# Kernel tuning notes

Measured on AMD Instinct MI355X. Metric: run time of the kernel, lower is better.

Reference implementation:

```python
import jax, jax.numpy as jnp
import numpy as np

HIDDEN = 2048
N_HEADS = 16
N_KV_HEADS = 4
HEAD_DIM = HIDDEN // N_HEADS  # 128
N_GROUPS = N_HEADS // N_KV_HEADS  # 4
ROPE_BASE = 10000.0


def rope_cos_sin(seq_len, dim, dtype=jnp.float32):
    inv_freq = 1.0 / (ROPE_BASE ** (jnp.arange(0, dim, 2, dtype=jnp.float32) / dim))
    t = jnp.arange(seq_len, dtype=jnp.float32)
    freqs = jnp.einsum('i,j->ij', t, inv_freq)          # [S, dim/2]
    emb = jnp.concatenate([freqs, freqs], axis=-1)       # [S, dim]
    return emb.astype(dtype).cos(), emb.astype(dtype).sin() if False else (jnp.cos(emb).astype(dtype), jnp.sin(emb).astype(dtype))[1] and None or (jnp.cos(emb).astype(dtype), jnp.sin(emb).astype(dtype))


def _rope_tables(seq_len, dim):
    inv_freq = 1.0 / (ROPE_BASE ** (jnp.arange(0, dim, 2, dtype=jnp.float32) / dim))
    t = jnp.arange(seq_len, dtype=jnp.float32)
    freqs = jnp.einsum('i,j->ij', t, inv_freq)
    emb = jnp.concatenate([freqs, freqs], axis=-1)
    return jnp.cos(emb), jnp.sin(emb)  # each [S, dim]


def rotate_half(x):
    d = x.shape[-1] // 2
    return jnp.concatenate([-x[..., d:], x[..., :d]], axis=-1)


def setup_inputs() -> dict:
    key = jax.random.key(0)
    ks = jax.random.split(key, 5)
    B, S = 2, 2048
    std = 0.02
    return {
        'hidden_states': jax.random.normal(ks[0], (B, S, HIDDEN), jnp.float32),
        'wq': jax.random.normal(ks[1], (HIDDEN, N_HEADS * HEAD_DIM), jnp.float32) * std,
        'wk': jax.random.normal(ks[2], (HIDDEN, N_KV_HEADS * HEAD_DIM), jnp.float32) * std,
        'wv': jax.random.normal(ks[3], (HIDDEN, N_KV_HEADS * HEAD_DIM), jnp.float32) * std,
        'wo': jax.random.normal(ks[4], (HIDDEN, HIDDEN), jnp.float32) * std,
    }


def reference(hidden_states, wq, wk, wv, wo):
    B, S, _ = hidden_states.shape
    q = (hidden_states @ wq).reshape(B, S, N_HEADS, HEAD_DIM)       # [B,S,Hq,D]
    k = (hidden_states @ wk).reshape(B, S, N_KV_HEADS, HEAD_DIM)    # [B,S,Hk,D]
    v = (hidden_states @ wv).reshape(B, S, N_KV_HEADS, HEAD_DIM)

    cos, sin = _rope_tables(S, HEAD_DIM)                            # [S,D]
    cos = cos[None, :, None, :]
    sin = sin[None, :, None, :]
    q = q * cos + rotate_half(q) * sin
    k = k * cos + rotate_half(k) * sin

    # GQA: repeat KV heads so kv head h maps to query heads h*G..h*G+G-1
    # (matches einops repeat 'b h s d -> b (h g) s d')
    k = jnp.repeat(k, N_GROUPS, axis=2)                              # [B,S,Hq,D]
    v = jnp.repeat(v, N_GROUPS, axis=2)

    scale = 1.0 / jnp.sqrt(jnp.asarray(HEAD_DIM, q.dtype))
    scores = jnp.einsum('bqhd,bkhd->bhqk', q, k) * scale            # [B,H,S,S]
    causal = jnp.triu(jnp.full((S, S), -jnp.inf, dtype=scores.dtype), k=1)
    scores = scores + causal
    probs = jax.nn.softmax(scores.astype(jnp.float32), axis=-1).astype(q.dtype)
    out = jnp.einsum('bhqk,bkhd->bqhd', probs, v)                   # [B,S,H,D]
    out = out.reshape(B, S, HIDDEN)
    return out @ wo
```

## Files before the change

kernel.cpp:

```cpp
#include <hip/hip_runtime.h>

#define HIDDEN 2048
#define NH 16
#define NKV 4
#define HD 128
#define BATCH 2
#define SEQ 2048
#define MROWS (BATCH*SEQ)
#define NQKV (NH*HD + 2*NKV*HD)
#define KOFF (NH*HD)
#define VOFF (NH*HD + NKV*HD)

typedef unsigned short u16;
typedef unsigned int u32;
typedef __bf16 bf16_t;
typedef bf16_t bf16x8 __attribute__((ext_vector_type(8)));
typedef float f32x4 __attribute__((ext_vector_type(4)));
typedef u16 u16x8 __attribute__((ext_vector_type(8)));

__device__ __forceinline__ u16 f2bf(float f) {
  u32 u = __builtin_bit_cast(u32, f);
  u32 r = (u + 0x7FFFu + ((u >> 16) & 1u)) >> 16;
  return (u16)r;
}
__device__ __forceinline__ float bf2f(u16 h) {
  u32 u = ((u32)h) << 16;
  return __builtin_bit_cast(float, u);
}

__global__ void cast_f32_bf16(const float* __restrict__ in, u16* __restrict__ out, int n8) {
  int i = blockIdx.x * blockDim.x + threadIdx.x;
  if (i >= n8) return;
  const float4* p = (const float4*)in + (size_t)i * 2;
  float4 a = p[0], b = p[1];
  u16x8 o;
  o[0]=f2bf(a.x); o[1]=f2bf(a.y); o[2]=f2bf(a.z); o[3]=f2bf(a.w);
  o[4]=f2bf(b.x); o[5]=f2bf(b.y); o[6]=f2bf(b.z); o[7]=f2bf(b.w);
  *((u16x8*)out + i) = o;
}

__global__ void transpose_cast(const float* __restrict__ src, u16* __restrict__ dst, int K, int N) {
  __shared__ float tile[32][33];
  int k0 = blockIdx.y * 32, n0 = blockIdx.x * 32;
  int tx = threadIdx.x, ty = threadIdx.y;
  #pragma unroll
  for (int j = 0; j < 32; j += 8)
    tile[ty + j][tx] = src[(size_t)(k0 + ty + j) * N + n0 + tx];
  __syncthreads();
  #pragma unroll
  for (int j = 0; j < 32; j += 8)
    dst[(size_t)(n0 + ty + j) * K + k0 + tx] = f2bf(tile[tx][ty + j]);
}

template<int OUT_BF16>
__global__ __launch_bounds__(256) void gemm_bt(const u16* __restrict__ A, const u16* __restrict__ Bt,
                                               void* __restrict__ Cout, int M, int N, int K) {
  __shared__ u16 As[2][128 * 32];
  __shared__ u16 Bs[2][128 * 32];
  const int tid = threadIdx.x;
  const int lane = tid & 63, wave = tid >> 6;
  const int mb = blockIdx.y * 128, nb = blockIdx.x * 128;
  const int wm = (wave >> 1) * 64, wn = (wave & 1) * 64;
  const int KT = K >> 5;

  auto stage = [&](int buf, int kt) {
    #pragma unroll
    for (int j = 0; j < 2; ++j) {
      int id0 = j * 256 + wave * 64;
      int id = id0 + lane;
      int row = id >> 2, c8 = (id & 3) * 8;
      const u16* ga = A + (size_t)(mb + row) * K + kt * 32 + c8;
      __builtin_amdgcn_global_load_lds((const __attribute__((address_space(1))) u32*)ga,
          (__attribute__((address_space(3))) u32*)&As[buf][id0 * 8], 16, 0, 0);
      const u16* gb = Bt + (size_t)(nb + row) * K + kt * 32 + c8;
      __builtin_amdgcn_global_load_lds((const __attribute__((address_space(1))) u32*)gb,
          (__attribute__((address_space(3))) u32*)&Bs[buf][id0 * 8], 16, 0, 0);
    }
  };

  f32x4 acc[4][4];
  #pragma unroll
  for (int i = 0; i < 4; ++i)
    #pragma unroll
    for (int j = 0; j < 4; ++j) acc[i][j] = (f32x4)0.0f;

  stage(0, 0);
  __syncthreads();
  for (int kt = 0; kt < KT; ++kt) {
    int cur = kt & 1;
    if (kt + 1 < KT) stage(cur ^ 1, kt + 1);
    bf16x8 af[4], bfr[4];
    #pragma unroll
    for (int mi = 0; mi < 4; ++mi) {
      int r = wm + mi * 16 + (lane & 15);
      af[mi] = __builtin_bit_cast(bf16x8, *(const u16x8*)&As[cur][r * 32 + (lane >> 4) * 8]);
    }
    #pragma unroll
    for (int ni = 0; ni < 4; ++ni) {
      int r = wn + ni * 16 + (lane & 15);
      bfr[ni] = __builtin_bit_cast(bf16x8, *(const u16x8*)&Bs[cur][r * 32 + (lane >> 4) * 8]);
    }
    #pragma unroll
    for (int mi = 0; mi < 4; ++mi)
      #pragma unroll
      for (int ni = 0; ni < 4; ++ni)
        acc[mi][ni] = __builtin_amdgcn_mfma_f32_16x16x32_bf16(af[mi], bfr[ni], acc[mi][ni], 0, 0, 0);
    __syncthreads();
  }
  int rbase = mb + wm + (lane >> 4) * 4;
  int cbase = nb + wn + (lane & 15);
  #pragma unroll
  for (int mi = 0; mi < 4; ++mi) {
    #pragma unroll
    for (int r = 0; r < 4; ++r) {
      int row = rbase + mi * 16 + r;
      #pragma unroll
      for (int ni = 0; ni < 4; ++ni) {
        int col = cbase + ni * 16;
        float v = acc[mi][ni][r];
        if (OUT_BF16) ((u16*)Cout)[(size_t)row * N + col] = f2bf(v);
        else          ((float*)Cout)[(size_t)row * N + col] = v;
      }
    }
  }
}

__global__ void rope_kernel(u16* __restrict__ qkv) {
  int idx = blockIdx.x * blockDim.x + threadIdx.x;
  int d = idx & 63;
  int t = idx >> 6;
  int hd = t % 20;
  int row = t / 20;
  int s = row & (SEQ - 1);
  int cb = (hd < NH) ? hd * HD : KOFF + (hd - NH) * HD;
  float inv = __expf((float)d * -0.14391156f);
  float freq = (float)s * inv;
  float sn = sinf(freq), cs = cosf(freq);
  size_t base = (size_t)row * NQKV + cb + d;
  float x0 = bf2f(qkv[base]), x1 = bf2f(qkv[base + 64]);
  qkv[base]      = f2bf(x0 * cs - x1 * sn);
  qkv[base + 64] = f2bf(x1 * cs + x0 * sn);
}

__global__ void vtrans_kernel(const u16* __restrict__ qkv, u16* __restrict__ vt) {
  __shared__ u16 tile[32][33];
  int bh = blockIdx.z;
  int d0 = blockIdx.y * 32;
  int s0 = blockIdx.x * 32;
  int b = bh >> 2, kvh = bh & 3;
  int tx = threadIdx.x, ty = threadIdx.y;
  const u16* src = qkv + (size_t)(b * SEQ) * NQKV + VOFF + kvh * HD;
  #pragma unroll
  for (int j = 0; j < 32; j += 8)
    tile[ty + j][tx] = src[(size_t)(s0 + ty + j) * NQKV + d0 + tx];
  __syncthreads();
  u16* dst = vt + (size_t)bh * HD * SEQ;
  #pragma unroll
  for (int j = 0; j < 32; j += 8)
    dst[(size_t)(d0 + ty + j) * SEQ + s0 + tx] = tile[tx][ty + j];
}

__global__ __launch_bounds__(512) void attn_kernel(const u16* __restrict__ qkv,
                                                   const u16* __restrict__ vt,
                                                   u16* __restrict__ out) {
  __shared__ u16 Ks[32 * 128];
  __shared__ u16 Vs[128 * 32];
  __shared__ u16 Ps[8][16 * 32];
  const int tid = threadIdx.x, lane = tid & 63, wave = tid >> 6;
  const int qt = blockIdx.x, h = blockIdx.y, b = blockIdx.z;
  const int kvh = h >> 2;
  const int q0 = qt * 128 + wave * 16;
  const float scale = 0.08838834764831845f;

  bf16x8 qf[4];
  {
    const u16* qp = qkv + (size_t)(b * SEQ + q0 + (lane & 15)) * NQKV + h * HD + (lane >> 4) * 8;
    #pragma unroll
    for (int kc = 0; kc < 4; ++kc)
      qf[kc] = __builtin_bit_cast(bf16x8, *(const u16x8*)(qp + kc * 32));
  }
  f32x4 oacc[8];
  #pragma unroll
  for (int i = 0; i < 8; ++i) oacc[i] = (f32x4)0.0f;
  float mrow[4], lrow[4];
  #pragma unroll
  for (int r = 0; r < 4; ++r) { mrow[r] = -INFINITY; lrow[r] = 0.0f; }

  const int ntiles = (qt + 1) * 4;
  const u16* kbase = qkv + (size_t)(b * SEQ) * NQKV + KOFF + kvh * HD;
  const u16* vbase = vt + (size_t)(b * NKV + kvh) * HD * SEQ;

  for (int t = 0; t < ntiles; ++t) {
    int kv0 = t * 32;
    {
      int row = tid >> 4, c8 = (tid & 15) * 8;
      u16x8 kd = *(const u16x8*)(kbase + (size_t)(kv0 + row) * NQKV + c8);
      int byte = (row * 256 + c8 * 2) ^ ((row & 7) << 4);
      *(u16x8*)((char*)Ks + byte) = kd;
      int vrow = tid >> 2, vc8 = (tid & 3) * 8;
      u16x8 vd = *(const u16x8*)(vbase + (size_t)vrow * SEQ + kv0 + vc8);
      int vbyte = (vrow * 64 + vc8 * 2) ^ ((vrow & 3) << 4);
      *(u16x8*)((char*)Vs + vbyte) = vd;
    }
    __syncthreads();
    if (kv0 <= q0 + 15) {
      f32x4 sacc[2];
      sacc[0] = (f32x4)0.0f; sacc[1] = (f32x4)0.0f;
      #pragma unroll
      for (int n2 = 0; n2 < 2; ++n2) {
        #pragma unroll
        for (int kc = 0; kc < 4; ++kc) {
          int kvr = n2 * 16 + (lane & 15);
          int byte = (kvr * 256 + (kc * 32 + (lane >> 4) * 8) * 2) ^ ((kvr & 7) << 4);
          bf16x8 kf = __builtin_bit_cast(bf16x8, *(const u16x8*)((const char*)Ks + byte));
          sacc[n2] = __builtin_amdgcn_mfma_f32_16x16x32_bf16(qf[kc], kf, sacc[n2], 0, 0, 0);
        }
      }
      int qrow_base = q0 + (lane >> 4) * 4;
      float pv[2][4];
      #pragma unroll
      for (int r = 0; r < 4; ++r) {
        int q = qrow_base + r;
        #pragma unroll
        for (int n2 = 0; n2 < 2; ++n2) {
          int kv = kv0 + n2 * 16 + (lane & 15);
          float sv = sacc[n2][r] * scale;
          pv[n2][r] = (kv <= q) ? sv : -INFINITY;
        }
        float v = fmaxf(pv[0][r], pv[1][r]);
        v = fmaxf(v, __shfl_xor(v, 1));
        v = fmaxf(v, __shfl_xor(v, 2));
        v = fmaxf(v, __shfl_xor(v, 4));
        v = fmaxf(v, __shfl_xor(v, 8));
        float mnew = fmaxf(mrow[r], v);
        float corr = __expf(mrow[r] - mnew);
        mrow[r] = mnew;
        float psum = 0.0f;
        #pragma unroll
        for (int n2 = 0; n2 < 2; ++n2) {
          float p = __expf(pv[n2][r] - mnew);
          pv[n2][r] = p;
          psum += p;
        }
        psum += __shfl_xor(psum, 1);
        psum += __shfl_xor(psum, 2);
        psum += __shfl_xor(psum, 4);
        psum += __shfl_xor(psum, 8);
        lrow[r] = lrow[r] * corr + psum;
        #pragma unroll
        for (int nt = 0; nt < 8; ++nt) oacc[nt][r] *= corr;
      }
      #pragma unroll
      for (int n2 = 0; n2 < 2; ++n2)
        #pragma unroll
        for (int r = 0; r < 4; ++r)
          Ps[wave][((lane >> 4) * 4 + r) * 32 + n2 * 16 + (lane & 15)] = f2bf(pv[n2][r]);
      asm volatile("s_waitcnt lgkmcnt(0)" ::: "memory");
      bf16x8 pf = __builtin_bit_cast(bf16x8, *(const u16x8*)&Ps[wave][(lane & 15) * 32 + (lane >> 4) * 8]);
      #pragma unroll
      for (int nt = 0; nt < 8; ++nt) {
        int d = nt * 16 + (lane & 15);
        int vbyte = (d * 64 + (lane >> 4) * 16) ^ ((d & 3) << 4);
        bf16x8 vf = __builtin_bit_cast(bf16x8, *(const u16x8*)((const char*)Vs + vbyte));
        oacc[nt] = __builtin_amdgcn_mfma_f32_16x16x32_bf16(pf, vf, oacc[nt], 0, 0, 0);
      }
    }
    __syncthreads();
  }
  #pragma unroll
  for (int nt = 0; nt < 8; ++nt) {
    #pragma unroll
    for (int r = 0; r < 4; ++r) {
      int row = b * SEQ + q0 + (lane >> 4) * 4 + r;
      int col = h * HD + nt * 16 + (lane & 15);
      out[(size_t)row * HIDDEN + col] = f2bf(oacc[nt][r] / lrow[r]);
    }
  }
}

extern "C" void kernel_launch(void* const* d_in, const int* in_sizes, int n_in,
                              void* d_out, int out_size, void* d_ws, size_t ws_size,
                              hipStream_t stream) {
  (void)in_sizes; (void)n_in; (void)out_size; (void)ws_size;
  const float* x  = (const float*)d_in[0];
  const float* wq = (const float*)d_in[1];
  const float* wk = (const float*)d_in[2];
  const float* wv = (const float*)d_in[3];
  const float* wo = (const float*)d_in[4];
  float* out = (float*)d_out;
  char* ws = (char*)d_ws;

  u16* xbf   = (u16*)(ws);
  u16* wqkvt = (u16*)(ws + (size_t)16777216);
  u16* wot   = (u16*)(ws + (size_t)16777216 + 12582912);
  u16* qkv   = (u16*)(ws + (size_t)16777216 + 12582912 + 8388608);
  u16* vtb   = (u16*)(ws + (size_t)16777216 + 12582912 + 8388608 + 25165824);
  u16* aout  = xbf;

  cast_f32_bf16<<<4096, 256, 0, stream>>>(x, xbf, MROWS * HIDDEN / 8);
  transpose_cast<<<dim3(64, 64), dim3(32, 8), 0, stream>>>(wq, wqkvt, HIDDEN, 2048);
  transpose_cast<<<dim3(16, 64), dim3(32, 8), 0, stream>>>(wk, wqkvt + (size_t)2048 * 2048, HIDDEN, 512);
  transpose_cast<<<dim3(16, 64), dim3(32, 8), 0, stream>>>(wv, wqkvt + (size_t)2560 * 2048, HIDDEN, 512);
  transpose_cast<<<dim3(64, 64), dim3(32, 8), 0, stream>>>(wo, wot, HIDDEN, HIDDEN);

  gemm_bt<1><<<dim3(NQKV / 128, MROWS / 128), 256, 0, stream>>>(xbf, wqkvt, qkv, MROWS, NQKV, HIDDEN);
  rope_kernel<<<(MROWS * 20 * 64) / 256, 256, 0, stream>>>(qkv);
  vtrans_kernel<<<dim3(SEQ / 32, HD / 32, BATCH * NKV), dim3(32, 8), 0, stream>>>(qkv, vtb);
  attn_kernel<<<dim3(SEQ / 128, NH, BATCH), 512, 0, stream>>>(qkv, vtb, aout);
  gemm_bt<0><<<dim3(HIDDEN / 128, MROWS / 128), 256, 0, stream>>>(aout, wot, out, MROWS, HIDDEN, HIDDEN);
}
```

Baseline: 432.9 us.

## Pair causal query tiles per block, double-buffer KV via direct LDS loads

Each attention block now handles two query tiles, qt and 15-qt, so causal work is balanced across blocks and each staged K/V tile is shared by both tiles. K/V tiles grow to 64 rows and are double-buffered in LDS using global_load_lds async copies with XOR swizzling, so the next tile loads while the current one is computed. The softmax rescale is skipped unless the row max rises by more than 8 (lazy rescaling). The costs are more registers for two accumulator sets, more LDS, and the grid halves to 256 blocks, which may lower occupancy.

```diff
diff --git a/kernel.cpp b/kernel.cpp
--- a/kernel.cpp
+++ b/kernel.cpp
@@ -163,117 +163,153 @@
 __global__ __launch_bounds__(512) void attn_kernel(const u16* __restrict__ qkv,
                                                    const u16* __restrict__ vt,
                                                    u16* __restrict__ out) {
-  __shared__ u16 Ks[32 * 128];
-  __shared__ u16 Vs[128 * 32];
-  __shared__ u16 Ps[8][16 * 32];
+  __shared__ u16 Ks[2][64 * 128];
+  __shared__ u16 Vs[2][128 * 64];
+  __shared__ u16 Ps[8][16 * 64];
   const int tid = threadIdx.x, lane = tid & 63, wave = tid >> 6;
-  const int qt = blockIdx.x, h = blockIdx.y, b = blockIdx.z;
+  const int qtA = blockIdx.x, qtB = 15 - qtA;
+  const int h = blockIdx.y, b = blockIdx.z;
   const int kvh = h >> 2;
-  const int q0 = qt * 128 + wave * 16;
+  const int q0A = qtA * 128 + wave * 16;
+  const int q0B = qtB * 128 + wave * 16;
   const float scale = 0.08838834764831845f;
 
-  bf16x8 qf[4];
-  {
-    const u16* qp = qkv + (size_t)(b * SEQ + q0 + (lane & 15)) * NQKV + h * HD + (lane >> 4) * 8;
-    #pragma unroll
-    for (int kc = 0; kc < 4; ++kc)
-      qf[kc] = __builtin_bit_cast(bf16x8, *(const u16x8*)(qp + kc * 32));
-  }
-  f32x4 oacc[8];
-  #pragma unroll
-  for (int i = 0; i < 8; ++i) oacc[i] = (f32x4)0.0f;
-  float mrow[4], lrow[4];
-  #pragma unroll
-  for (int r = 0; r < 4; ++r) { mrow[r] = -INFINITY; lrow[r] = 0.0f; }
-
-  const int ntiles = (qt + 1) * 4;
   const u16* kbase = qkv + (size_t)(b * SEQ) * NQKV + KOFF + kvh * HD;
   const u16* vbase = vt + (size_t)(b * NKV + kvh) * HD * SEQ;
 
-  for (int t = 0; t < ntiles; ++t) {
-    int kv0 = t * 32;
-    {
-      int row = tid >> 4, c8 = (tid & 15) * 8;
-      u16x8 kd = *(const u16x8*)(kbase + (size_t)(kv0 + row) * NQKV + c8);
-      int byte = (row * 256 + c8 * 2) ^ ((row & 7) << 4);
-      *(u16x8*)((char*)Ks + byte) = kd;
-      int vrow = tid >> 2, vc8 = (tid & 3) * 8;
-      u16x8 vd = *(const u16x8*)(vbase + (size_t)vrow * SEQ + kv0 + vc8);
-      int vbyte = (vrow * 64 + vc8 * 2) ^ ((vrow & 3) << 4);
-      *(u16x8*)((char*)Vs + vbyte) = vd;
-    }
-    __syncthreads();
-    if (kv0 <= q0 + 15) {
-      f32x4 sacc[2];
-      sacc[0] = (f32x4)0.0f; sacc[1] = (f32x4)0.0f;
+  bf16x8 qfA[4], qfB[4];
+  {
+    const u16* qa = qkv + (size_t)(b * SEQ + q0A + (lane & 15)) * NQKV + h * HD + (lane >> 4) * 8;
+    const u16* qb = qkv + (size_t)(b * SEQ + q0B + (lane & 15)) * NQKV + h * HD + (lane >> 4) * 8;
+    #pragma unroll
+    for (int kc = 0; kc < 4; ++kc) {
+      qfA[kc] = __builtin_bit_cast(bf16x8, *(const u16x8*)(qa + kc * 32));
+      qfB[kc] = __builtin_bit_cast(bf16x8, *(const u16x8*)(qb + kc * 32));
+    }
+  }
+  f32x4 oaccA[8], oaccB[8];
+  float mA[4], lA[4], mB[4], lB[4];
+  #pragma unroll
+  for (int i = 0; i < 8; ++i) { oaccA[i] = (f32x4)0.0f; oaccB[i] = (f32x4)0.0f; }
+  #pragma unroll
+  for (int r = 0; r < 4; ++r) { mA[r] = -INFINITY; lA[r] = 0.0f; mB[r] = -INFINITY; lB[r] = 0.0f; }
+
+  auto stage = [&](int buf, int t) {
+    int kv0 = t * 64;
+    #pragma unroll
+    for (int j = 0; j < 2; ++j) {
+      int kvr = wave * 8 + j * 4 + (lane >> 4);
+      int sc = (lane & 15) ^ (kvr & 7);
+      const u16* src = kbase + (size_t)(kv0 + kvr) * NQKV + sc * 8;
+      __builtin_amdgcn_global_load_lds((const __attribute__((address_space(1))) u32*)src,
+          (__attribute__((address_space(3))) u32*)&Ks[buf][(wave * 8 + j * 4) * 128], 16, 0, 0);
+    }
+    #pragma unroll
+    for (int j = 0; j < 2; ++j) {
+      int d = wave * 16 + j * 8 + (lane >> 3);
+      int sc = (lane & 7) ^ (d & 7);
+      const u16* src = vbase + (size_t)d * SEQ + kv0 + sc * 8;
+      __builtin_amdgcn_global_load_lds((const __attribute__((address_space(1))) u32*)src,
+          (__attribute__((address_space(3))) u32*)&Vs[buf][(wave * 16 + j * 8) * 64], 16, 0, 0);
+    }
+  };
+
+  auto do_ctx = [&](const bf16x8 (&qf)[4], f32x4 (&oacc)[8], float (&mr)[4], float (&lr)[4],
+                    int q0c, int kv0, int cur) {
+    f32x4 sacc[4];
+    #pragma unroll
+    for (int n2 = 0; n2 < 4; ++n2) sacc[n2] = (f32x4)0.0f;
+    #pragma unroll
+    for (int n2 = 0; n2 < 4; ++n2) {
+      int kvr = n2 * 16 + (lane & 15);
       #pragma unroll
-      for (int n2 = 0; n2 < 2; ++n2) {
-        #pragma unroll
-        for (int kc = 0; kc < 4; ++kc) {
-          int kvr = n2 * 16 + (lane & 15);
-          int byte = (kvr * 256 + (kc * 32 + (lane >> 4) * 8) * 2) ^ ((kvr & 7) << 4);
-          bf16x8 kf = __builtin_bit_cast(bf16x8, *(const u16x8*)((const char*)Ks + byte));
-          sacc[n2] = __builtin_amdgcn_mfma_f32_16x16x32_bf16(qf[kc], kf, sacc[n2], 0, 0, 0);
-        }
-      }
-      int qrow_base = q0 + (lane >> 4) * 4;
-      float pv[2][4];
-      #pragma unroll
-      for (int r = 0; r < 4; ++r) {
-        int q = qrow_base + r;
-        #pragma unroll
-        for (int n2 = 0; n2 < 2; ++n2) {
-          int kv = kv0 + n2 * 16 + (lane & 15);
-          float sv = sacc[n2][r] * scale;
-          pv[n2][r] = (kv <= q) ? sv : -INFINITY;
-        }
-        float v = fmaxf(pv[0][r], pv[1][r]);
-        v = fmaxf(v, __shfl_xor(v, 1));
-        v = fmaxf(v, __shfl_xor(v, 2));
-        v = fmaxf(v, __shfl_xor(v, 4));
-        v = fmaxf(v, __shfl_xor(v, 8));
-        float mnew = fmaxf(mrow[r], v);
-        float corr = __expf(mrow[r] - mnew);
-        mrow[r] = mnew;
-        float psum = 0.0f;
-        #pragma unroll
-        for (int n2 = 0; n2 < 2; ++n2) {
-          float p = __expf(pv[n2][r] - mnew);
-          pv[n2][r] = p;
-          psum += p;
-        }
-        psum += __shfl_xor(psum, 1);
-        psum += __shfl_xor(psum, 2);
-        psum += __shfl_xor(psum, 4);
-        psum += __shfl_xor(psum, 8);
-        lrow[r] = lrow[r] * corr + psum;
+      for (int kc = 0; kc < 4; ++kc) {
+        int ch = (kc * 4 + (lane >> 4)) ^ (kvr & 7);
+        bf16x8 kf = __builtin_bit_cast(bf16x8, *(const u16x8*)&Ks[cur][kvr * 128 + ch * 8]);
+        sacc[n2] = __builtin_amdgcn_mfma_f32_16x16x32_bf16(qf[kc], kf, sacc[n2], 0, 0, 0);
+      }
+    }
+    u16* pwb = &Ps[wave][0];
+    #pragma unroll
+    for (int r = 0; r < 4; ++r) {
+      int qr = (lane >> 4) * 4 + r;
+      int q = q0c + qr;
+      float p0, p1, p2, p3;
+      {
+        int kvc = kv0 + (lane & 15);
+        p0 = (kvc       <= q) ? sacc[0][r] * scale : -INFINITY;
+        p1 = (kvc + 16  <= q) ? sacc[1][r] * scale : -INFINITY;
+        p2 = (kvc + 32  <= q) ? sacc[2][r] * scale : -INFINITY;
+        p3 = (kvc + 48  <= q) ? sacc[3][r] * scale : -INFINITY;
+      }
+      float v = fmaxf(fmaxf(p0, p1), fmaxf(p2, p3));
+      v = fmaxf(v, __shfl_xor(v, 1));
+      v = fmaxf(v, __shfl_xor(v, 2));
+      v = fmaxf(v, __shfl_xor(v, 4));
+      v = fmaxf(v, __shfl_xor(v, 8));
+      float m = mr[r];
+      if (v > m + 8.0f) {
+        float corr = __expf(m - v);
+        lr[r] *= corr;
         #pragma unroll
         for (int nt = 0; nt < 8; ++nt) oacc[nt][r] *= corr;
-      }
+        m = v; mr[r] = v;
+      }
+      float e0 = __expf(p0 - m), e1 = __expf(p1 - m);
+      float e2 = __expf(p2 - m), e3 = __expf(p3 - m);
+      float ps = (e0 + e1) + (e2 + e3);
+      ps += __shfl_xor(ps, 1);
+      ps += __shfl_xor(ps, 2);
+      ps += __shfl_xor(ps, 4);
+      ps += __shfl_xor(ps, 8);
+      lr[r] += ps;
+      char* base = (char*)pwb + qr * 128 + (lane & 7) * 2;
+      int half = (lane & 15) >> 3;
+      *(u16*)(base + (((0 + half) ^ (qr & 7)) << 4)) = f2bf(e0);
+      *(u16*)(base + (((2 + half) ^ (qr & 7)) << 4)) = f2bf(e1);
+      *(u16*)(base + (((4 + half) ^ (qr & 7)) << 4)) = f2bf(e2);
+      *(u16*)(base + (((6 + half) ^ (qr & 7)) << 4)) = f2bf(e3);
+    }
+    asm volatile("s_waitcnt lgkmcnt(0)" ::: "memory");
+    bf16x8 pf[2];
+    #pragma unroll
+    for (int k2 = 0; k2 < 2; ++k2) {
+      int q = lane & 15;
+      int ch = (k2 * 4 + (lane >> 4)) ^ (q & 7);
+      pf[k2] = __builtin_bit_cast(bf16x8, *(const u16x8*)((const char*)pwb + q * 128 + ch * 16));
+    }
+    #pragma unroll
+    for (int nt = 0; nt < 8; ++nt) {
+      int d = nt * 16 + (lane & 15);
       #pragma unroll
-      for (int n2 = 0; n2 < 2; ++n2)
-        #pragma unroll
-        for (int r = 0; r < 4; ++r)
-          Ps[wave][((lane >> 4) * 4 + r) * 32 + n2 * 16 + (lane & 15)] = f2bf(pv[n2][r]);
-      asm volatile("s_waitcnt lgkmcnt(0)" ::: "memory");
-      bf16x8 pf = __builtin_bit_cast(bf16x8, *(const u16x8*)&Ps[wave][(lane & 15) * 32 + (lane >> 4) * 8]);
-      #pragma unroll
-      for (int nt = 0; nt < 8; ++nt) {
-        int d = nt * 16 + (lane & 15);
-        int vbyte = (d * 64 + (lane >> 4) * 16) ^ ((d & 3) << 4);
-        bf16x8 vf = __builtin_bit_cast(bf16x8, *(const u16x8*)((const char*)Vs + vbyte));
-        oacc[nt] = __builtin_amdgcn_mfma_f32_16x16x32_bf16(pf, vf, oacc[nt], 0, 0, 0);
-      }
-    }
+      for (int k2 = 0; k2 < 2; ++k2) {
+        int ch = (k2 * 4 + (lane >> 4)) ^ (d & 7);
+        bf16x8 vf = __builtin_bit_cast(bf16x8, *(const u16x8*)&Vs[cur][d * 64 + ch * 8]);
+        oacc[nt] = __builtin_amdgcn_mfma_f32_16x16x32_bf16(pf[k2], vf, oacc[nt], 0, 0, 0);
+      }
+    }
+  };
+
+  const int nt_tiles = (qtB + 1) * 2;
+  stage(0, 0);
+  __syncthreads();
+  for (int t = 0; t < nt_tiles; ++t) {
+    int cur = t & 1;
+    if (t + 1 < nt_tiles) stage(cur ^ 1, t + 1);
+    int kv0 = t * 64;
+    if (kv0 <= q0A + 15) do_ctx(qfA, oaccA, mA, lA, q0A, kv0, cur);
+    if (kv0 <= q0B + 15) do_ctx(qfB, oaccB, mB, lB, q0B, kv0, cur);
     __syncthreads();
   }
   #pragma unroll
   for (int nt = 0; nt < 8; ++nt) {
     #pragma unroll
     for (int r = 0; r < 4; ++r) {
-      int row = b * SEQ + q0 + (lane >> 4) * 4 + r;
       int col = h * HD + nt * 16 + (lane & 15);
-      out[(size_t)row * HIDDEN + col] = f2bf(oacc[nt][r] / lrow[r]);
+      int rowA = b * SEQ + q0A + (lane >> 4) * 4 + r;
+      int rowB = b * SEQ + q0B + (lane >> 4) * 4 + r;
+      out[(size_t)rowA * HIDDEN + col] = f2bf(oaccA[nt][r] / lA[r]);
+      out[(size_t)rowB * HIDDEN + col] = f2bf(oaccB[nt][r] / lB[r]);
     }
   }
 }
@@ -306,6 +342,6 @@
   gemm_bt<1><<<dim3(NQKV / 128, MROWS / 128), 256, 0, stream>>>(xbf, wqkvt, qkv, MROWS, NQKV, HIDDEN);
   rope_kernel<<<(MROWS * 20 * 64) / 256, 256, 0, stream>>>(qkv);
   vtrans_kernel<<<dim3(SEQ / 32, HD / 32, BATCH * NKV), dim3(32, 8), 0, stream>>>(qkv, vtb);
-  attn_kernel<<<dim3(SEQ / 128, NH, BATCH), 512, 0, stream>>>(qkv, vtb, aout);
+  attn_kernel<<<dim3(8, NH, BATCH), 512, 0, stream>>>(qkv, vtb, aout);
   gemm_bt<0><<<dim3(HIDDEN / 128, MROWS / 128), 256, 0, stream>>>(aout, wot, out, MROWS, HIDDEN, HIDDEN);
 }
```

Measured after the change: 375.5 us. 13.3% less time.
